# Kernel optimization log

Hardware: AMD Instinct MI355X
Metric: run time of the kernel (lower is better)

The kernel has to match this reference:

```python
import jax, jax.numpy as jnp
import numpy as np

B, N, FIN, H, F = 8, 1024, 256, 8, 64
NEG_SLOPE = 0.2


def setup_inputs() -> dict:
    key = jax.random.key(0)
    k = jax.random.split(key, 6)
    x = jax.random.normal(k[0], (B, N, FIN), dtype=jnp.float32)
    adj_mask = jax.random.randint(k[1], (B, N, N), 0, 2, dtype=jnp.int32)
    edge_prior = jax.random.normal(k[2], (B, N, N), dtype=jnp.float32)
    # params (xavier-style scales)
    W = jax.random.normal(k[3], (FIN, H * F), dtype=jnp.float32) * np.sqrt(2.0 / (FIN + H * F))
    a_left = jax.random.normal(k[4], (H, F), dtype=jnp.float32) * np.sqrt(2.0 / (1 + F))
    a_right = jax.random.normal(k[5], (H, F), dtype=jnp.float32) * np.sqrt(2.0 / (1 + F))
    edge_scale = jnp.float32(0.05)
    return {"x": x, "adj_mask": adj_mask, "edge_prior": edge_prior,
            "W": W, "a_left": a_left, "a_right": a_right, "edge_scale": edge_scale}


def reference(x, adj_mask, edge_prior, W, a_left, a_right, edge_scale):
    b, n, _ = x.shape
    h = (x @ W).reshape(b, n, H, F)                      # [B,N,H,F]
    e_left = jnp.einsum('bnhf,hf->bnh', h, a_left)       # [B,N,H]
    e_right = jnp.einsum('bnhf,hf->bnh', h, a_right)     # [B,N,H]
    e = jax.nn.leaky_relu(e_left[:, :, None, :] + e_right[:, None, :, :],
                          negative_slope=NEG_SLOPE)      # [B,N,N,H]
    e = e + edge_scale * edge_prior[..., None]
    e = jnp.where((adj_mask == 0)[..., None], -jnp.inf, e)
    alpha = jax.nn.softmax(e, axis=2)                    # softmax over neighbors j
    h_new = jnp.einsum('bijh,bjhf->bihf', alpha, h)      # [B,N,H,F]
    return h_new.reshape(b, n, H * F)                    # concat=True
```

## Files before the change

### kernel.cpp

```cpp
#include <hip/hip_runtime.h>
#include <hip/hip_bf16.h>

#define B_ 8
#define N_ 1024
#define FIN_ 256
#define H_ 8
#define F_ 64
#define HF_ 512
#define BN_ 8192
#define LOG2E 1.4426950408889634f

using bf16x8 = __attribute__((ext_vector_type(8))) short;
using f32x4  = __attribute__((ext_vector_type(4))) float;
using i32x4  = __attribute__((ext_vector_type(4))) int;

__device__ __forceinline__ short f2bf(float x) {
  __hip_bfloat16 b = __float2bfloat16(x);
  return *reinterpret_cast<short*>(&b);
}
__device__ __forceinline__ float bf2f(short s) {
  union { unsigned u; float f; } v;
  v.u = ((unsigned)(unsigned short)s) << 16;
  return v.f;
}
__device__ __forceinline__ bf16x8 cvtCE(f32x4 pa, f32x4 pb, i32x4 ma, i32x4 mb, float es) {
  bf16x8 o;
#pragma unroll
  for (int e = 0; e < 4; e++) {
    o[e]     = f2bf(ma[e] != 0 ? es * pa[e] : -1e30f);
    o[e + 4] = f2bf(mb[e] != 0 ? es * pb[e] : -1e30f);
  }
  return o;
}

__global__ __launch_bounds__(256) void k_cvt(
    const float* __restrict__ x, const float* __restrict__ W,
    short* __restrict__ xb, short* __restrict__ Wt) {
  const int bid = blockIdx.x;
  if (bid < 1024) {
    const int idx = (bid * 256 + threadIdx.x) * 8;
    f32x4 a = *(const f32x4*)(x + idx);
    f32x4 b = *(const f32x4*)(x + idx + 4);
    bf16x8 o;
    o[0]=f2bf(a[0]); o[1]=f2bf(a[1]); o[2]=f2bf(a[2]); o[3]=f2bf(a[3]);
    o[4]=f2bf(b[0]); o[5]=f2bf(b[1]); o[6]=f2bf(b[2]); o[7]=f2bf(b[3]);
    *(bf16x8*)(xb + idx) = o;
  } else {
    const int idx = (bid - 1024) * 256 + threadIdx.x;
    const int f = idx >> 8, c = idx & 255;
    Wt[f * FIN_ + c] = f2bf(W[c * HF_ + f]);
  }
}

__global__ __launch_bounds__(256) void k_h(
    const short* __restrict__ Wt, const short* __restrict__ xb,
    const float* __restrict__ aL, const float* __restrict__ aR,
    short* __restrict__ hA, float* __restrict__ el_t, float* __restrict__ er_t) {
  const int nt = blockIdx.x;
  const int h  = blockIdx.y;
  const int w  = threadIdx.x >> 6;
  const int l  = threadIdx.x & 63;
  const int lr = l & 15, lk = l >> 4;
  const int n0 = nt * 64;
  const int fbase = h * 64 + w * 16;

  f32x4 acc[4] = {};
  const short* arow = Wt + (fbase + lr) * FIN_ + lk * 8;

#pragma unroll
  for (int k0 = 0; k0 < FIN_; k0 += 32) {
    bf16x8 a = *(const bf16x8*)(arow + k0);
#pragma unroll
    for (int nf = 0; nf < 4; nf++) {
      bf16x8 bb = *(const bf16x8*)(xb + (size_t)(n0 + nf * 16 + lr) * FIN_ + k0 + lk * 8);
      acc[nf] = __builtin_amdgcn_mfma_f32_16x16x32_bf16(a, bb, acc[nf], 0, 0, 0);
    }
  }

  __shared__ short sT[64][72];
  __shared__ float sEl[4][64], sEr[4][64];
  float al[4], ar[4];
#pragma unroll
  for (int r = 0; r < 4; r++) {
    const int fl = w * 16 + lk * 4 + r;
    al[r] = aL[h * F_ + fl];
    ar[r] = aR[h * F_ + fl];
  }
#pragma unroll
  for (int nf = 0; nf < 4; nf++) {
    const int nl = nf * 16 + lr;
#pragma unroll
    for (int r = 0; r < 4; r++)
      sT[w * 16 + lk * 4 + r][nl] = f2bf(acc[nf][r]);
    float pl = acc[nf][0]*al[0] + acc[nf][1]*al[1] + acc[nf][2]*al[2] + acc[nf][3]*al[3];
    float pr = acc[nf][0]*ar[0] + acc[nf][1]*ar[1] + acc[nf][2]*ar[2] + acc[nf][3]*ar[3];
    pl += __shfl_xor(pl, 16); pl += __shfl_xor(pl, 32);
    pr += __shfl_xor(pr, 16); pr += __shfl_xor(pr, 32);
    if (lk == 0) { sEl[w][nl] = pl; sEr[w][nl] = pr; }
  }
  __syncthreads();
  if (threadIdx.x < 64) {
    const int n = threadIdx.x;
    el_t[h * BN_ + n0 + n] = (sEl[0][n] + sEl[1][n] + sEl[2][n] + sEl[3][n]) * LOG2E;
    er_t[h * BN_ + n0 + n] = (sEr[0][n] + sEr[1][n] + sEr[2][n] + sEr[3][n]) * LOG2E;
  }
  const int b8h = (nt >> 4) * 8 + h;
  const int jb  = (nt & 15) * 2;
#pragma unroll
  for (int gi = 0; gi < 2; gi++) {
    const int g   = threadIdx.x * 2 + gi;
    const int jsl = g >> 8, ff = (g >> 6) & 3, gl = g & 63;
    const int glr = gl & 15, glk = gl >> 4;
    bf16x8 v = *(const bf16x8*)(&sT[ff * 16 + glr][jsl * 32 + glk * 8]);
    *(bf16x8*)(hA + (((size_t)b8h * 32 + jb + jsl) * 4 + ff) * 512 + gl * 8) = v;
  }
}

__global__ __launch_bounds__(512, 4) void k_attn(
    const short* __restrict__ hA, const float* __restrict__ el_t,
    const float* __restrict__ er_t, const float* __restrict__ prior,
    const int* __restrict__ mask, const float* __restrict__ esp,
    float* __restrict__ out) {
  const int bid = blockIdx.x;
  const int b  = bid & 7;
  const int it = bid >> 3;
  const int t  = threadIdx.x;
  const int h  = t >> 6;
  const int l  = t & 63;
  const int lr = l & 15, lk = l >> 4;
  const int i0 = it * 16;
  const size_t bn = (size_t)b * N_;
  const float es = esp[0] * LOG2E;

  __shared__ short cbuf[16 * 1024];

  {
    const int srow = t >> 5, cg0 = t & 31;
    const int sw = srow & 7;
    const size_t grow = (bn + i0 + srow) * (size_t)N_;
    const float* pg = prior + grow;
    const int*   mg = mask  + grow;
#pragma unroll
    for (int k = 0; k < 4; k++) {
      const int g = cg0 + 32 * k;
      f32x4 p0 = *(const f32x4*)(pg + g * 8), p1 = *(const f32x4*)(pg + g * 8 + 4);
      i32x4 m0 = *(const i32x4*)(mg + g * 8), m1 = *(const i32x4*)(mg + g * 8 + 4);
      *(bf16x8*)(&cbuf[srow * 1024 + (g ^ sw) * 8]) = cvtCE(p0, p1, m0, m1, es);
    }
  }

  const float el = el_t[h * BN_ + bn + i0 + lr];
  const float* erp = er_t + h * BN_ + bn + lk * 8;
  const short* hW  = hA + (size_t)(b * 8 + h) * 65536 + l * 8;
  const short* cbl = cbuf + lr * 1024;
  const int xsw = lr & 7;

  bf16x8 hC[4], hN[4];
#pragma unroll
  for (int ff = 0; ff < 4; ff++) hC[ff] = *(const bf16x8*)(hW + ff * 512);

  __syncthreads();

  bf16x8 cC = *(const bf16x8*)(cbl + (lk ^ xsw) * 8);
  f32x4 acc[4] = {};
  f32x4 accS = {};
  bf16x8 ones;
#pragma unroll
  for (int e = 0; e < 8; e++) ones[e] = (short)0x3F80;

  for (int s = 0; s < 32; ++s) {
    const int sn = (s < 31) ? s + 1 : 31;
    const short* hs = hW + (size_t)sn * 2048;
    hN[0] = *(const bf16x8*)(hs);
    hN[1] = *(const bf16x8*)(hs + 512);
    hN[2] = *(const bf16x8*)(hs + 1024);
    hN[3] = *(const bf16x8*)(hs + 1536);
    bf16x8 cN = *(const bf16x8*)(cbl + (((sn * 4 + lk) ^ xsw) * 8));
    f32x4 er0 = *(const f32x4*)(erp + s * 32);
    f32x4 er1 = *(const f32x4*)(erp + s * 32 + 4);

    bf16x8 pf;
#pragma unroll
    for (int q = 0; q < 4; q++) {
      float sA = el + er0[q];
      float vA = fmaf(0.6f, sA, bf2f(cC[q]));
      vA = fmaf(0.4f, fabsf(sA), vA);
      float sB = el + er1[q];
      float vB = fmaf(0.6f, sB, bf2f(cC[q + 4]));
      vB = fmaf(0.4f, fabsf(sB), vB);
      float x1, x2;
      asm("v_exp_f32 %0, %1" : "=v"(x1) : "v"(vA));
      asm("v_exp_f32 %0, %1" : "=v"(x2) : "v"(vB));
      pf[q] = f2bf(x1); pf[q + 4] = f2bf(x2);
    }
    accS   = __builtin_amdgcn_mfma_f32_16x16x32_bf16(ones, pf, accS, 0, 0, 0);
    acc[0] = __builtin_amdgcn_mfma_f32_16x16x32_bf16(hC[0], pf, acc[0], 0, 0, 0);
    acc[1] = __builtin_amdgcn_mfma_f32_16x16x32_bf16(hC[1], pf, acc[1], 0, 0, 0);
    acc[2] = __builtin_amdgcn_mfma_f32_16x16x32_bf16(hC[2], pf, acc[2], 0, 0, 0);
    acc[3] = __builtin_amdgcn_mfma_f32_16x16x32_bf16(hC[3], pf, acc[3], 0, 0, 0);
#pragma unroll
    for (int ff = 0; ff < 4; ff++) hC[ff] = hN[ff];
    cC = cN;
  }

  const float inv = 1.0f / accS[0];
  const size_t row = bn + i0 + lr;
#pragma unroll
  for (int ff = 0; ff < 4; ff++) {
    f32x4 v = acc[ff];
    v[0] *= inv; v[1] *= inv; v[2] *= inv; v[3] *= inv;
    *(f32x4*)(out + row * HF_ + h * 64 + ff * 16 + lk * 4) = v;
  }
}

extern "C" void kernel_launch(void* const* d_in, const int* in_sizes, int n_in,
                              void* d_out, int out_size, void* d_ws, size_t ws_size,
                              hipStream_t stream) {
  const float* x     = (const float*)d_in[0];
  const int*   adj   = (const int*)  d_in[1];
  const float* prior = (const float*)d_in[2];
  const float* W     = (const float*)d_in[3];
  const float* aL    = (const float*)d_in[4];
  const float* aR    = (const float*)d_in[5];
  const float* es    = (const float*)d_in[6];
  float* out = (float*)d_out;

  char* ws = (char*)d_ws;
  short* hA   = (short*)ws;
  short* xb   = (short*)(ws + 8u  * 1024 * 1024);
  short* Wt   = (short*)(ws + 12u * 1024 * 1024);
  float* el_t = (float*)(ws + 12u * 1024 * 1024 + 262144);
  float* er_t = (float*)(ws + 12u * 1024 * 1024 + 524288);

  hipLaunchKernelGGL(k_cvt, dim3(1536), dim3(256), 0, stream, x, W, xb, Wt);
  hipLaunchKernelGGL(k_h,   dim3(128, 8), dim3(256), 0, stream,
                     Wt, xb, aL, aR, hA, el_t, er_t);
  hipLaunchKernelGGL(k_attn, dim3(512), dim3(512), 0, stream,
                     hA, el_t, er_t, prior, adj, es, out);
}
```

Measured before the change: 70.74 us.

## Split attention heads across two blocks and double-buffer the neighbor loop

The attention kernel now uses 256-thread blocks that each handle four heads, so twice as many blocks cover the same rows. The main loop is manually unrolled by two with ping-pong register buffers, so prefetches of h, edge terms and e_right run ahead of the compute. Each block still builds the full 16x1024 edge-bias tile in shared memory. That means the prior and mask rows are now read and converted twice per row tile, which adds global memory traffic in exchange for more blocks and better latency hiding.

New measurement: 68.84 us. -2.7%, faster.

```diff
diff --git a/kernel.cpp b/kernel.cpp
--- a/kernel.cpp
+++ b/kernel.cpp
@@ -116,16 +116,52 @@
   }
 }
 
-__global__ __launch_bounds__(512, 4) void k_attn(
+#define PREF_(sn, Hd, Cd, E0d, E1d)                                   \
+  {                                                                   \
+    const short* hs_ = hW + (size_t)(sn) * 2048;                      \
+    Hd[0] = *(const bf16x8*)(hs_);                                    \
+    Hd[1] = *(const bf16x8*)(hs_ + 512);                              \
+    Hd[2] = *(const bf16x8*)(hs_ + 1024);                             \
+    Hd[3] = *(const bf16x8*)(hs_ + 1536);                             \
+    Cd    = *(const bf16x8*)(cbl + (((sn) * 4 + lk) ^ xsw) * 8);      \
+    E0d   = *(const f32x4*)(erp + (sn) * 32);                         \
+    E1d   = *(const f32x4*)(erp + (sn) * 32 + 4);                     \
+  }
+
+#define COMP_(Hu, Cu, E0u, E1u)                                               \
+  {                                                                           \
+    bf16x8 pf;                                                                \
+    _Pragma("unroll")                                                         \
+    for (int q = 0; q < 4; q++) {                                             \
+      float sA = el + E0u[q];                                                 \
+      float vA = fmaf(0.6f, sA, bf2f(Cu[q]));                                 \
+      vA = fmaf(0.4f, fabsf(sA), vA);                                         \
+      float sB = el + E1u[q];                                                 \
+      float vB = fmaf(0.6f, sB, bf2f(Cu[q + 4]));                             \
+      vB = fmaf(0.4f, fabsf(sB), vB);                                         \
+      float x1_, x2_;                                                         \
+      asm("v_exp_f32 %0, %1" : "=v"(x1_) : "v"(vA));                          \
+      asm("v_exp_f32 %0, %1" : "=v"(x2_) : "v"(vB));                          \
+      pf[q] = f2bf(x1_); pf[q + 4] = f2bf(x2_);                               \
+    }                                                                         \
+    accS   = __builtin_amdgcn_mfma_f32_16x16x32_bf16(ones, pf, accS, 0, 0, 0);\
+    acc[0] = __builtin_amdgcn_mfma_f32_16x16x32_bf16(Hu[0], pf, acc[0], 0,0,0);\
+    acc[1] = __builtin_amdgcn_mfma_f32_16x16x32_bf16(Hu[1], pf, acc[1], 0,0,0);\
+    acc[2] = __builtin_amdgcn_mfma_f32_16x16x32_bf16(Hu[2], pf, acc[2], 0,0,0);\
+    acc[3] = __builtin_amdgcn_mfma_f32_16x16x32_bf16(Hu[3], pf, acc[3], 0,0,0);\
+  }
+
+__global__ __launch_bounds__(256, 4) void k_attn(
     const short* __restrict__ hA, const float* __restrict__ el_t,
     const float* __restrict__ er_t, const float* __restrict__ prior,
     const int* __restrict__ mask, const float* __restrict__ esp,
     float* __restrict__ out) {
   const int bid = blockIdx.x;
   const int b  = bid & 7;
-  const int it = bid >> 3;
+  const int hp = (bid >> 3) & 1;
+  const int it = bid >> 4;
   const int t  = threadIdx.x;
-  const int h  = t >> 6;
+  const int h  = hp * 4 + (t >> 6);
   const int l  = t & 63;
   const int lr = l & 15, lk = l >> 4;
   const int i0 = it * 16;
@@ -135,14 +171,15 @@
   __shared__ short cbuf[16 * 1024];
 
   {
-    const int srow = t >> 5, cg0 = t & 31;
-    const int sw = srow & 7;
+    const int srow = t >> 4;
+    const int cg0  = t & 15;
+    const int sw   = srow & 7;
     const size_t grow = (bn + i0 + srow) * (size_t)N_;
     const float* pg = prior + grow;
     const int*   mg = mask  + grow;
 #pragma unroll
-    for (int k = 0; k < 4; k++) {
-      const int g = cg0 + 32 * k;
+    for (int k = 0; k < 8; k++) {
+      const int g = cg0 + 16 * k;
       f32x4 p0 = *(const f32x4*)(pg + g * 8), p1 = *(const f32x4*)(pg + g * 8 + 4);
       i32x4 m0 = *(const i32x4*)(mg + g * 8), m1 = *(const i32x4*)(mg + g * 8 + 4);
       *(bf16x8*)(&cbuf[srow * 1024 + (g ^ sw) * 8]) = cvtCE(p0, p1, m0, m1, es);
@@ -155,52 +192,31 @@
   const short* cbl = cbuf + lr * 1024;
   const int xsw = lr & 7;
 
-  bf16x8 hC[4], hN[4];
-#pragma unroll
-  for (int ff = 0; ff < 4; ff++) hC[ff] = *(const bf16x8*)(hW + ff * 512);
-
-  __syncthreads();
-
-  bf16x8 cC = *(const bf16x8*)(cbl + (lk ^ xsw) * 8);
+  bf16x8 hA_[4], hB_[4], cA_, cB_;
+  f32x4 eA0, eA1, eB0, eB1;
+
+  hA_[0] = *(const bf16x8*)(hW);
+  hA_[1] = *(const bf16x8*)(hW + 512);
+  hA_[2] = *(const bf16x8*)(hW + 1024);
+  hA_[3] = *(const bf16x8*)(hW + 1536);
+  eA0 = *(const f32x4*)(erp);
+  eA1 = *(const f32x4*)(erp + 4);
+
   f32x4 acc[4] = {};
   f32x4 accS = {};
   bf16x8 ones;
 #pragma unroll
   for (int e = 0; e < 8; e++) ones[e] = (short)0x3F80;
 
-  for (int s = 0; s < 32; ++s) {
-    const int sn = (s < 31) ? s + 1 : 31;
-    const short* hs = hW + (size_t)sn * 2048;
-    hN[0] = *(const bf16x8*)(hs);
-    hN[1] = *(const bf16x8*)(hs + 512);
-    hN[2] = *(const bf16x8*)(hs + 1024);
-    hN[3] = *(const bf16x8*)(hs + 1536);
-    bf16x8 cN = *(const bf16x8*)(cbl + (((sn * 4 + lk) ^ xsw) * 8));
-    f32x4 er0 = *(const f32x4*)(erp + s * 32);
-    f32x4 er1 = *(const f32x4*)(erp + s * 32 + 4);
-
-    bf16x8 pf;
-#pragma unroll
-    for (int q = 0; q < 4; q++) {
-      float sA = el + er0[q];
-      float vA = fmaf(0.6f, sA, bf2f(cC[q]));
-      vA = fmaf(0.4f, fabsf(sA), vA);
-      float sB = el + er1[q];
-      float vB = fmaf(0.6f, sB, bf2f(cC[q + 4]));
-      vB = fmaf(0.4f, fabsf(sB), vB);
-      float x1, x2;
-      asm("v_exp_f32 %0, %1" : "=v"(x1) : "v"(vA));
-      asm("v_exp_f32 %0, %1" : "=v"(x2) : "v"(vB));
-      pf[q] = f2bf(x1); pf[q + 4] = f2bf(x2);
-    }
-    accS   = __builtin_amdgcn_mfma_f32_16x16x32_bf16(ones, pf, accS, 0, 0, 0);
-    acc[0] = __builtin_amdgcn_mfma_f32_16x16x32_bf16(hC[0], pf, acc[0], 0, 0, 0);
-    acc[1] = __builtin_amdgcn_mfma_f32_16x16x32_bf16(hC[1], pf, acc[1], 0, 0, 0);
-    acc[2] = __builtin_amdgcn_mfma_f32_16x16x32_bf16(hC[2], pf, acc[2], 0, 0, 0);
-    acc[3] = __builtin_amdgcn_mfma_f32_16x16x32_bf16(hC[3], pf, acc[3], 0, 0, 0);
-#pragma unroll
-    for (int ff = 0; ff < 4; ff++) hC[ff] = hN[ff];
-    cC = cN;
+  __syncthreads();
+  cA_ = *(const bf16x8*)(cbl + ((lk ^ xsw) * 8));
+
+  for (int s = 0; s < 32; s += 2) {
+    PREF_(s + 1, hB_, cB_, eB0, eB1);
+    COMP_(hA_, cA_, eA0, eA1);
+    const int s2 = (s + 2 < 32) ? s + 2 : 31;
+    PREF_(s2, hA_, cA_, eA0, eA1);
+    COMP_(hB_, cB_, eB0, eB1);
   }
 
   const float inv = 1.0f / accS[0];
@@ -235,6 +251,6 @@
   hipLaunchKernelGGL(k_cvt, dim3(1536), dim3(256), 0, stream, x, W, xb, Wt);
   hipLaunchKernelGGL(k_h,   dim3(128, 8), dim3(256), 0, stream,
                      Wt, xb, aL, aR, hA, el_t, er_t);
-  hipLaunchKernelGGL(k_attn, dim3(512), dim3(512), 0, stream,
+  hipLaunchKernelGGL(k_attn, dim3(1024), dim3(256), 0, stream,
                      hA, el_t, er_t, prior, adj, es, out);
 }
```
